# Optimization experiments

Hardware: AMD Instinct MI355X
Metric: run time of the kernel (lower is better)

The kernel has to match this reference:

```python
import jax, jax.numpy as jnp
import numpy as np

IN_SHAPE = 640
LEVELS = [3, 4, 5]          # pyramid_levels [3,5] expanded
REG_LEN = 64
NUM_CLASSES = 80
MAX_OUT = 100
SCORE_TH = 0.3
IOU_TH = 0.5
NEG_INF = -1e30


def _make_anchors():
    """Anchor-free anchors: one box per grid cell, grid_zero_start=True,
    anchor_scale=1, aspect_ratio=1 -> half-size = stride/2. Normalized by input size."""
    all_a = []
    for lvl in LEVELS:
        stride = 2 ** lvl
        fs = IN_SHAPE // stride
        hh = np.arange(fs, dtype='float32') * stride
        ww = np.arange(fs, dtype='float32') * stride
        wg, hg = np.meshgrid(ww, hh)
        centers = np.stack([hg, wg], -1).reshape(-1, 2)  # [fs*fs, 2] (h, w)
        half = stride * 0.5
        all_a.append(np.concatenate([centers - half, centers + half], -1))
    return np.concatenate(all_a, 0) / IN_SHAPE  # [8400, 4]


def setup_inputs() -> dict:
    key = jax.random.key(0)
    preds = jax.random.normal(key, (64, 8400, REG_LEN + NUM_CLASSES), dtype=jnp.float32)
    anchors = jnp.asarray(_make_anchors(), dtype=jnp.float32)
    return {"preds": preds, "anchors": anchors}


def _decode_yolov8(preds, anchors):
    bbox_logits, cls_logits = preds[..., :REG_LEN], preds[..., REG_LEN:]
    B, N = bbox_logits.shape[:2]
    bins = REG_LEN // 4  # 16
    d = bbox_logits.reshape(B, N, 4, bins)
    # softmax-weighted DFL expectation over bins
    d = jnp.sum(jax.nn.softmax(d, axis=-1) * jnp.arange(bins, dtype=d.dtype), axis=-1)  # [B,N,4]
    tl, br = d[..., :2], d[..., 2:]
    anchors_hw = anchors[:, 2:] - anchors[:, :2]          # [N,2]
    anchors_ctr = (anchors[:, :2] + anchors[:, 2:]) * 0.5  # [N,2]
    bc = (br - tl) * 0.5 * anchors_hw + anchors_ctr        # center
    bhw = (br + tl) * anchors_hw                           # height/width
    boxes = jnp.concatenate([bc - bhw * 0.5, bc + bhw * 0.5], -1)  # [B,N,4] corners
    return boxes, cls_logits


def _iou_one_vs_all(box, boxes):
    tl = jnp.maximum(box[:2], boxes[:, :2])
    br = jnp.minimum(box[2:], boxes[:, 2:])
    inter = jnp.prod(jnp.clip(br - tl, 0.0, None), -1)
    a1 = jnp.prod(box[2:] - box[:2])
    a2 = jnp.prod(boxes[:, 2:] - boxes[:, :2], -1)
    return inter / (a1 + a2 - inter + 1e-9)


def _nms_single(boxes, scores):
    """Greedy hard NMS for one image. boxes [N,4], scores [N] -> idxs [MAX_OUT] (-1 = invalid)."""
    n = scores.shape[0]
    sc0 = jnp.where(scores > SCORE_TH, scores, NEG_INF)

    def step(sc, _):
        j = jnp.argmax(sc)
        valid = sc[j] > NEG_INF * 0.5
        idx = jnp.where(valid, j, -1).astype(jnp.int32)
        iou = _iou_one_vs_all(boxes[j], boxes)
        sc = jnp.where((iou > IOU_TH) | (jnp.arange(n) == j), NEG_INF, sc)
        return sc, idx

    _, idxs = jax.lax.scan(step, sc0, None, length=MAX_OUT)
    return idxs


def reference(preds, anchors):
    boxes, cls = _decode_yolov8(preds, anchors)       # [B,N,4], [B,N,C]
    scores = jnp.max(cls, -1)                          # [B,N]
    labels = jnp.argmax(cls, -1).astype(jnp.int32)     # [B,N]
    idxs = jax.vmap(_nms_single)(boxes, scores)        # [B,MAX_OUT]
    valid = idxs >= 0
    safe = jnp.maximum(idxs, 0)
    out_boxes = jnp.take_along_axis(boxes, safe[:, :, None], axis=1) * valid[..., None]
    out_scores = jnp.take_along_axis(scores, safe, axis=1) * valid
    out_labels = jnp.where(valid, jnp.take_along_axis(labels, safe, axis=1), -1)
    return out_boxes, out_labels, out_scores
```

## Files before the change

### kernel.cpp

```cpp
#include <hip/hip_runtime.h>

namespace {
constexpr int kB = 64;
constexpr int kN = 8400;
constexpr int kNP = 16384;
constexpr int kReg = 64;
constexpr int kCls = 80;
constexpr int kStride = kReg + kCls;
constexpr int kMaxOut = 100;
constexpr float kScoreTh = 0.3f;
constexpr float kIouTh = 0.5f;
}

__global__ __launch_bounds__(256) void decode_k(
    const float* __restrict__ preds,
    const float* __restrict__ anchors,
    float4* __restrict__ boxes,
    float* __restrict__ scores,
    int* __restrict__ labels)
{
    int idx = blockIdx.x * blockDim.x + threadIdx.x;
    if (idx >= kB * kN) return;
    int n = idx - (idx / kN) * kN;
    const float* p = preds + (size_t)idx * kStride;

    float d[4];
#pragma unroll
    for (int s = 0; s < 4; ++s) {
        float x[16];
        const float4* q = (const float4*)(p + s * 16);
#pragma unroll
        for (int j = 0; j < 4; ++j) ((float4*)x)[j] = q[j];
        float m = x[0];
#pragma unroll
        for (int j = 1; j < 16; ++j) m = fmaxf(m, x[j]);
        float se = 0.f, we = 0.f;
#pragma unroll
        for (int j = 0; j < 16; ++j) {
            float t = expf(x[j] - m);
            se += t;
            we += t * (float)j;
        }
        d[s] = we / se;
    }

    float4 a = ((const float4*)anchors)[n];
    float ah0 = a.z - a.x, ah1 = a.w - a.y;
    float c0 = (a.x + a.z) * 0.5f, c1 = (a.y + a.w) * 0.5f;
    float bc0 = (d[2] - d[0]) * 0.5f * ah0 + c0;
    float bc1 = (d[3] - d[1]) * 0.5f * ah1 + c1;
    float bh0 = (d[2] + d[0]) * ah0;
    float bh1 = (d[3] + d[1]) * ah1;
    boxes[idx] = make_float4(bc0 - bh0 * 0.5f, bc1 - bh1 * 0.5f,
                             bc0 + bh0 * 0.5f, bc1 + bh1 * 0.5f);

    const float4* cl = (const float4*)(p + kReg);
    float best = -3e38f; int bl = 0;
#pragma unroll
    for (int c = 0; c < kCls / 4; ++c) {
        float4 v = cl[c];
        if (v.x > best) { best = v.x; bl = 4 * c + 0; }
        if (v.y > best) { best = v.y; bl = 4 * c + 1; }
        if (v.z > best) { best = v.z; bl = 4 * c + 2; }
        if (v.w > best) { best = v.w; bl = 4 * c + 3; }
    }
    scores[idx] = best;
    labels[idx] = bl;
}

__global__ __launch_bounds__(256) void keys_k(
    const float* __restrict__ scores, unsigned long long* __restrict__ keys)
{
    int t = blockIdx.x * 256 + threadIdx.x;
    int b = t >> 14, i = t & (kNP - 1);
    unsigned long long k = ~0ULL;
    if (i < kN) {
        float s = scores[b * kN + i];
        if (s > kScoreTh) {
            unsigned u = __float_as_uint(s);
            unsigned o = u ^ ((u & 0x80000000u) ? 0xFFFFFFFFu : 0x80000000u);
            k = ((unsigned long long)(~o) << 32) | (unsigned)i;
        }
    }
    keys[t] = k;
}

__global__ __launch_bounds__(512) void sortB_k(unsigned long long* __restrict__ keys)
{
    __shared__ unsigned long long lk[8192];
    const int h = blockIdx.x & 1;
    unsigned long long* base = keys + ((size_t)blockIdx.x << 13);
    for (int t = threadIdx.x; t < 8192; t += 512) lk[t] = base[t];
    __syncthreads();
    for (int size = 2; size <= 8192; size <<= 1) {
        const bool isTop = (size == 8192);
        for (int stride = size >> 1; stride > 0; stride >>= 1) {
#pragma unroll
            for (int p = 0; p < 8; ++p) {
                int n = threadIdx.x + (p << 9);
                int i = ((n & ~(stride - 1)) << 1) | (n & (stride - 1));
                int j = i + stride;
                bool desc = isTop ? (h == 1) : ((i & size) != 0);
                unsigned long long a = lk[i], c = lk[j];
                bool sw = desc ? (c > a) : (a > c);
                if (sw) { lk[i] = c; lk[j] = a; }
            }
            __syncthreads();
        }
    }
    for (int t = threadIdx.x; t < 8192; t += 512) base[t] = lk[t];
}

__global__ __launch_bounds__(256) void sortC_k(unsigned long long* __restrict__ keys)
{
    int t = blockIdx.x * 256 + threadIdx.x;
    int b = t >> 13, i = t & 8191;
    unsigned long long* p = keys + ((size_t)b << 14);
    unsigned long long a = p[i], c = p[i + 8192];
    if (a > c) { p[i] = c; p[i + 8192] = a; }
}

__global__ __launch_bounds__(512) void sortD_k(unsigned long long* __restrict__ keys)
{
    __shared__ unsigned long long lk[8192];
    unsigned long long* base = keys + ((size_t)blockIdx.x << 13);
    for (int t = threadIdx.x; t < 8192; t += 512) lk[t] = base[t];
    __syncthreads();
    for (int stride = 4096; stride > 0; stride >>= 1) {
#pragma unroll
        for (int p = 0; p < 8; ++p) {
            int n = threadIdx.x + (p << 9);
            int i = ((n & ~(stride - 1)) << 1) | (n & (stride - 1));
            int j = i + stride;
            unsigned long long a = lk[i], c = lk[j];
            if (a > c) { lk[i] = c; lk[j] = a; }
        }
        __syncthreads();
    }
    for (int t = threadIdx.x; t < 8192; t += 512) base[t] = lk[t];
}

__global__ __launch_bounds__(256) void nms_k(
    const float4* __restrict__ boxes,
    const float* __restrict__ scores,
    const int* __restrict__ labels,
    const unsigned long long* __restrict__ keys,
    float* __restrict__ out)
{
    __shared__ float4 kbox[kMaxOut];
    __shared__ float karea[kMaxOut];
    __shared__ unsigned long long ball[4];
    __shared__ int firstt, kcS, doneS, stopS;

    const int b = blockIdx.x, tid = threadIdx.x;
    const unsigned long long* sk = keys + ((size_t)b << 14);
    const float4* bx = boxes + (size_t)b * kN;

    if (tid == 0) { kcS = 0; doneS = 0; }

    for (int c = 0; c < kNP / 256; ++c) {
        __syncthreads();
        if (tid == 0) stopS = (sk[c * 256] == ~0ULL);
        unsigned long long key = sk[c * 256 + tid];
        bool alive = (key != ~0ULL);
        int idx = alive ? (int)(key & 0xFFFFFFFFULL) : 0;
        float4 cb = bx[idx];
        float ac = (cb.z - cb.x) * (cb.w - cb.y);
        __syncthreads();
        if (stopS) break;
        int kcl = kcS;
        if (alive) {
            for (int k = 0; k < kcl; ++k) {
                float4 kb = kbox[k];
                float t0 = fmaxf(kb.x, cb.x), t1 = fmaxf(kb.y, cb.y);
                float b0 = fminf(kb.z, cb.z), b1 = fminf(kb.w, cb.w);
                float inter = fmaxf(b0 - t0, 0.f) * fmaxf(b1 - t1, 0.f);
                float iou = inter / (karea[k] + ac - inter + 1e-9f);
                if (iou > kIouTh) { alive = false; break; }
            }
        }
        while (true) {
            unsigned long long m = __ballot((int)alive);
            if ((tid & 63) == 0) ball[tid >> 6] = m;
            __syncthreads();
            if (tid == 0) {
                int ft = -1;
                for (int w = 0; w < 4; ++w)
                    if (ball[w]) { ft = (w << 6) + __ffsll(ball[w]) - 1; break; }
                firstt = ft;
            }
            __syncthreads();
            int ft = firstt;
            if (ft < 0) break;
            if (tid == ft) {
                int k = kcS;
                kbox[k] = cb; karea[k] = ac;
                ((float4*)out)[b * kMaxOut + k] = cb;
                out[kB * kMaxOut * 4 + b * kMaxOut + k] =
                    (float)labels[(size_t)b * kN + idx];
                out[kB * kMaxOut * 5 + b * kMaxOut + k] =
                    scores[(size_t)b * kN + idx];
                kcS = k + 1;
                alive = false;
                if (k + 1 == kMaxOut) doneS = 1;
            }
            __syncthreads();
            if (doneS) break;
            int kn = kcS;
            if (alive) {
                float4 kb = kbox[kn - 1];
                float t0 = fmaxf(kb.x, cb.x), t1 = fmaxf(kb.y, cb.y);
                float b0 = fminf(kb.z, cb.z), b1 = fminf(kb.w, cb.w);
                float inter = fmaxf(b0 - t0, 0.f) * fmaxf(b1 - t1, 0.f);
                float iou = inter / (karea[kn - 1] + ac - inter + 1e-9f);
                if (iou > kIouTh) alive = false;
            }
            __syncthreads();
        }
        if (doneS) break;
    }
    __syncthreads();
    int kcf = kcS;
    for (int k = kcf + tid; k < kMaxOut; k += 256) {
        ((float4*)out)[b * kMaxOut + k] = make_float4(0.f, 0.f, 0.f, 0.f);
        out[kB * kMaxOut * 4 + b * kMaxOut + k] = -1.0f;
        out[kB * kMaxOut * 5 + b * kMaxOut + k] = 0.0f;
    }
}

extern "C" void kernel_launch(void* const* d_in, const int* in_sizes, int n_in,
                              void* d_out, int out_size, void* d_ws, size_t ws_size,
                              hipStream_t stream)
{
    const float* preds = (const float*)d_in[0];
    const float* anchors = (const float*)d_in[1];
    float* out = (float*)d_out;

    char* ws = (char*)d_ws;
    float4* boxes = (float4*)ws;
    float* scores = (float*)(ws + (size_t)kB * kN * 16);
    int* labels = (int*)(ws + (size_t)kB * kN * 20);
    unsigned long long* keys =
        (unsigned long long*)(ws + (size_t)kB * kN * 24);

    int total = kB * kN;
    decode_k<<<(total + 255) / 256, 256, 0, stream>>>(preds, anchors, boxes, scores, labels);
    keys_k<<<(kB * kNP) / 256, 256, 0, stream>>>(scores, keys);
    sortB_k<<<kB * 2, 512, 0, stream>>>(keys);
    sortC_k<<<(kB * 8192) / 256, 256, 0, stream>>>(keys);
    sortD_k<<<kB * 2, 512, 0, stream>>>(keys);
    nms_k<<<kB, 256, 0, stream>>>(boxes, scores, labels, keys, out);
}
```

Measured before the change: 608.8 us.

## Fuse key generation into decode with LDS-staged coalesced loads and 4-thread anchors

Replaces the one-thread-per-anchor decode with a block that stages 64 anchor rows into padded LDS using coalesced float4 loads. Four threads then split each anchor's DFL sides and class ranges and combine results with wave shuffles. The sort-key generation kernel is folded into this decode, saving one launch and a scores round trip. Padding keys are now produced inside the first sort stage instead of being written to memory. The intent is to fix the strided, uncoalesced 576-byte-per-thread reads, at the cost of more LDS use per block.

Result: no change. 603.8 us (-0.8%).

```diff
diff --git a/kernel.cpp b/kernel.cpp
--- a/kernel.cpp
+++ b/kernel.cpp
@@ -12,77 +12,98 @@
 constexpr float kIouTh = 0.5f;
 }
 
-__global__ __launch_bounds__(256) void decode_k(
+__global__ __launch_bounds__(256) void decode2_k(
     const float* __restrict__ preds,
     const float* __restrict__ anchors,
     float4* __restrict__ boxes,
     float* __restrict__ scores,
-    int* __restrict__ labels)
-{
-    int idx = blockIdx.x * blockDim.x + threadIdx.x;
-    if (idx >= kB * kN) return;
-    int n = idx - (idx / kN) * kN;
-    const float* p = preds + (size_t)idx * kStride;
-
-    float d[4];
-#pragma unroll
-    for (int s = 0; s < 4; ++s) {
-        float x[16];
-        const float4* q = (const float4*)(p + s * 16);
-#pragma unroll
-        for (int j = 0; j < 4; ++j) ((float4*)x)[j] = q[j];
-        float m = x[0];
-#pragma unroll
-        for (int j = 1; j < 16; ++j) m = fmaxf(m, x[j]);
-        float se = 0.f, we = 0.f;
-#pragma unroll
-        for (int j = 0; j < 16; ++j) {
-            float t = expf(x[j] - m);
-            se += t;
-            we += t * (float)j;
-        }
-        d[s] = we / se;
-    }
-
-    float4 a = ((const float4*)anchors)[n];
-    float ah0 = a.z - a.x, ah1 = a.w - a.y;
-    float c0 = (a.x + a.z) * 0.5f, c1 = (a.y + a.w) * 0.5f;
-    float bc0 = (d[2] - d[0]) * 0.5f * ah0 + c0;
-    float bc1 = (d[3] - d[1]) * 0.5f * ah1 + c1;
-    float bh0 = (d[2] + d[0]) * ah0;
-    float bh1 = (d[3] + d[1]) * ah1;
-    boxes[idx] = make_float4(bc0 - bh0 * 0.5f, bc1 - bh1 * 0.5f,
-                             bc0 + bh0 * 0.5f, bc1 + bh1 * 0.5f);
-
-    const float4* cl = (const float4*)(p + kReg);
-    float best = -3e38f; int bl = 0;
-#pragma unroll
-    for (int c = 0; c < kCls / 4; ++c) {
+    int* __restrict__ labels,
+    unsigned long long* __restrict__ keys)
+{
+    __shared__ float lds[64 * 148];
+    const int tid = threadIdx.x;
+    const size_t gbase = (size_t)blockIdx.x * 64;
+
+    const float4* src = (const float4*)(preds + gbase * kStride);
+    float4* l4 = (float4*)lds;
+#pragma unroll
+    for (int k = 0; k < 9; ++k) {
+        int i = tid + k * 256;
+        int row = i / 36, col = i - row * 36;
+        l4[row * 37 + col] = src[i];
+    }
+    __syncthreads();
+
+    const int a = tid >> 2, s = tid & 3;
+    const float* rowp = lds + a * 148;
+
+    float x[16];
+    const float4* q = (const float4*)(rowp + s * 16);
+#pragma unroll
+    for (int j = 0; j < 4; ++j) ((float4*)x)[j] = q[j];
+    float m = x[0];
+#pragma unroll
+    for (int j = 1; j < 16; ++j) m = fmaxf(m, x[j]);
+    float se = 0.f, we = 0.f;
+#pragma unroll
+    for (int j = 0; j < 16; ++j) {
+        float t = expf(x[j] - m);
+        se += t;
+        we += t * (float)j;
+    }
+    float d = we / se;
+
+    const float4* cl = (const float4*)(rowp + kReg + s * 20);
+    float bv = -3e38f; int bi = 0;
+#pragma unroll
+    for (int c = 0; c < 5; ++c) {
         float4 v = cl[c];
-        if (v.x > best) { best = v.x; bl = 4 * c + 0; }
-        if (v.y > best) { best = v.y; bl = 4 * c + 1; }
-        if (v.z > best) { best = v.z; bl = 4 * c + 2; }
-        if (v.w > best) { best = v.w; bl = 4 * c + 3; }
-    }
-    scores[idx] = best;
-    labels[idx] = bl;
-}
-
-__global__ __launch_bounds__(256) void keys_k(
-    const float* __restrict__ scores, unsigned long long* __restrict__ keys)
-{
-    int t = blockIdx.x * 256 + threadIdx.x;
-    int b = t >> 14, i = t & (kNP - 1);
-    unsigned long long k = ~0ULL;
-    if (i < kN) {
-        float s = scores[b * kN + i];
-        if (s > kScoreTh) {
-            unsigned u = __float_as_uint(s);
+        int cb = s * 20 + 4 * c;
+        if (v.x > bv) { bv = v.x; bi = cb; }
+        if (v.y > bv) { bv = v.y; bi = cb + 1; }
+        if (v.z > bv) { bv = v.z; bi = cb + 2; }
+        if (v.w > bv) { bv = v.w; bi = cb + 3; }
+    }
+
+    const int lane = tid & 63;
+    const int base = lane & ~3;
+    float d0 = __shfl(d, base + 0, 64);
+    float d1 = __shfl(d, base + 1, 64);
+    float d2 = __shfl(d, base + 2, 64);
+    float d3 = __shfl(d, base + 3, 64);
+    float v1 = __shfl(bv, base + 1, 64); int i1 = __shfl(bi, base + 1, 64);
+    float v2 = __shfl(bv, base + 2, 64); int i2 = __shfl(bi, base + 2, 64);
+    float v3 = __shfl(bv, base + 3, 64); int i3 = __shfl(bi, base + 3, 64);
+
+    if (s == 0) {
+        float best = bv; int bl = bi;
+        if (v1 > best) { best = v1; bl = i1; }
+        if (v2 > best) { best = v2; bl = i2; }
+        if (v3 > best) { best = v3; bl = i3; }
+
+        size_t gi = gbase + a;
+        int bimg = (int)(gi / kN);
+        int n = (int)(gi - (size_t)bimg * kN);
+        float4 av = ((const float4*)anchors)[n];
+        float ah0 = av.z - av.x, ah1 = av.w - av.y;
+        float c0 = (av.x + av.z) * 0.5f, c1 = (av.y + av.w) * 0.5f;
+        float bc0 = (d2 - d0) * 0.5f * ah0 + c0;
+        float bc1 = (d3 - d1) * 0.5f * ah1 + c1;
+        float bh0 = (d2 + d0) * ah0;
+        float bh1 = (d3 + d1) * ah1;
+        boxes[gi] = make_float4(bc0 - bh0 * 0.5f, bc1 - bh1 * 0.5f,
+                                bc0 + bh0 * 0.5f, bc1 + bh1 * 0.5f);
+        scores[gi] = best;
+        labels[gi] = bl;
+
+        unsigned long long kkey = ~0ULL;
+        if (best > kScoreTh) {
+            unsigned u = __float_as_uint(best);
             unsigned o = u ^ ((u & 0x80000000u) ? 0xFFFFFFFFu : 0x80000000u);
-            k = ((unsigned long long)(~o) << 32) | (unsigned)i;
-        }
-    }
-    keys[t] = k;
+            kkey = ((unsigned long long)(~o) << 32) | (unsigned)n;
+        }
+        keys[((size_t)bimg << 14) + n] = kkey;
+    }
 }
 
 __global__ __launch_bounds__(512) void sortB_k(unsigned long long* __restrict__ keys)
@@ -90,7 +111,8 @@
     __shared__ unsigned long long lk[8192];
     const int h = blockIdx.x & 1;
     unsigned long long* base = keys + ((size_t)blockIdx.x << 13);
-    for (int t = threadIdx.x; t < 8192; t += 512) lk[t] = base[t];
+    for (int t = threadIdx.x; t < 8192; t += 512)
+        lk[t] = (h * 8192 + t < kN) ? base[t] : ~0ULL;
     __syncthreads();
     for (int size = 2; size <= 8192; size <<= 1) {
         const bool isTop = (size == 8192);
@@ -180,8 +202,8 @@
             }
         }
         while (true) {
-            unsigned long long m = __ballot((int)alive);
-            if ((tid & 63) == 0) ball[tid >> 6] = m;
+            unsigned long long mm = __ballot((int)alive);
+            if ((tid & 63) == 0) ball[tid >> 6] = mm;
             __syncthreads();
             if (tid == 0) {
                 int ft = -1;
@@ -243,9 +265,7 @@
     unsigned long long* keys =
         (unsigned long long*)(ws + (size_t)kB * kN * 24);
 
-    int total = kB * kN;
-    decode_k<<<(total + 255) / 256, 256, 0, stream>>>(preds, anchors, boxes, scores, labels);
-    keys_k<<<(kB * kNP) / 256, 256, 0, stream>>>(scores, keys);
+    decode2_k<<<(kB * kN) / 64, 256, 0, stream>>>(preds, anchors, boxes, scores, labels, keys);
     sortB_k<<<kB * 2, 512, 0, stream>>>(keys);
     sortC_k<<<(kB * 8192) / 256, 256, 0, stream>>>(keys);
     sortD_k<<<kB * 2, 512, 0, stream>>>(keys);
```
